# Performance work log

Hardware: AMD Instinct MI355X
Metric: run time of the kernel (lower is better)

## Reference

```python
import jax, jax.numpy as jnp
import numpy as np

N, M, F, W = 600000, 300000, 128, 256  # points, masked points, grid feat_dim, net width


def _lin_init(k, fi, fo):
    k1, k2 = jax.random.split(k)
    s = 1.0 / np.sqrt(fi)
    return (jax.random.uniform(k1, (fi, fo), jnp.float32, -s, s),
            jax.random.uniform(k2, (fo,), jnp.float32, -s, s))


def setup_inputs() -> dict:
    key = jax.random.key(0)
    ks = jax.random.split(key, 24)
    # unique sorted indices emulate the boolean target_mask (static count M)
    idx = jnp.asarray(np.sort(np.random.RandomState(0).permutation(N)[:M]).astype(np.int32))
    inp = {
        "rays_pts_emb": jax.random.normal(ks[0], (N, 3), jnp.float32),
        "rotations_emb": jax.random.normal(ks[1], (N, 4), jnp.float32),
        "shs_emb": jax.random.normal(ks[2], (N, 16, 3), jnp.float32),
        "time_emb": jax.random.uniform(ks[3], (N, 1), jnp.float32),
        "h_emb": jax.random.uniform(ks[4], (N, 1), jnp.float32),
        "grid_sp": jax.random.normal(ks[5], (M, F), jnp.float32),
        "grid_st": jax.random.normal(ks[6], (M, F), jnp.float32),
        "idx": idx,
    }
    layers = [("sp", F, W), ("st", F, W), ("p1", W, W), ("p2", W, 9),
              ("r1", W, W), ("r2", W, 4), ("s1", W, W), ("s2", W, 48),
              ("w1", W, W), ("w2", W, 1), ("m1", W, W), ("m2", W, 1)]
    for i, (nm, fi, fo) in enumerate(layers):
        Wt, b = _lin_init(ks[7 + i], fi, fo)
        inp["W_" + nm] = Wt
        inp["b_" + nm] = b
    return inp


def _head(x, W1, b1, W2, b2):
    # nn.Sequential(ReLU, Linear, ReLU, Linear)
    h = jax.nn.relu(x)
    h = jax.nn.relu(h @ W1 + b1)
    return h @ W2 + b2


def reference(rays_pts_emb, rotations_emb, shs_emb, time_emb, h_emb, grid_sp, grid_st, idx,
              W_sp, b_sp, W_st, b_st, W_p1, b_p1, W_p2, b_p2, W_r1, b_r1, W_r2, b_r2,
              W_s1, b_s1, W_s2, b_s2, W_w1, b_w1, W_w2, b_w2, W_m1, b_m1, W_m2, b_m2):
    # encoders (Linear only, no activation)
    sp = grid_sp @ W_sp + b_sp            # [M, W]
    st = grid_st @ W_st + b_st            # [M, W]
    t = time_emb[0:1]                     # [1, 1]
    mint = 1.0 - t
    # position deformation: Bezier combination of 3 control offsets
    dx = _head(sp, W_p1, b_p1, W_p2, b_p2).reshape(-1, 3, 3)  # [M, 3, 3]
    delta = (3.0 * mint ** 2 * t * dx[:, 0]
             + 3.0 * mint * t ** 2 * dx[:, 1]
             + t ** 3 * dx[:, 2])                              # [M, 3]
    pts = rays_pts_emb.at[idx].add(delta)
    rotations = rotations_emb.at[idx].add(_head(st, W_r1, b_r1, W_r2, b_r2))
    shs = shs_emb.at[idx].add(_head(st, W_s1, b_s1, W_s2, b_s2).reshape(-1, 16, 3))
    # opacity gating
    w = _head(sp, W_w1, b_w1, W_w2, b_w2) ** 2                 # [M, 1]
    mu = jax.nn.sigmoid(_head(sp, W_m1, b_m1, W_m2, b_m2))     # [M, 1]
    opacity = h_emb.at[idx].set(h_emb[idx] * jnp.exp(-w * (t - mu) ** 2))
    return (pts, rotations, opacity, shs)
```

## Files before the change

### kernel.cpp

```cpp
#include <hip/hip_runtime.h>
#include <hip/hip_bf16.h>
#include <stdint.h>

#define M_ROWS 300000

typedef __attribute__((ext_vector_type(8)))  short bf16x8;
typedef __attribute__((ext_vector_type(16))) float f32x16;

union U4 { uint4 u; bf16x8 h; unsigned short us[8]; };

__device__ __forceinline__ unsigned short f2bf(float f) {
  union { float f; uint32_t u; } v; v.f = f;
  uint32_t r = v.u + 0x7fffu + ((v.u >> 16) & 1u);
  return (unsigned short)(r >> 16);
}
__device__ __forceinline__ uint32_t pk2(float lo, float hi) {
  return (uint32_t)f2bf(lo) | ((uint32_t)f2bf(hi) << 16);
}

#define T_SP 0
#define T_ST 64
#define T_P1 128
#define T_P2 256
#define T_R1 272
#define T_R2 400
#define T_S1 416
#define T_S2 544
#define T_W1 576
#define T_W2 704
#define T_M1 720
#define T_M2 848
#define T_TOT 864

__global__ void prep_w(const float* Wsp, const float* Wst, const float* Wp1, const float* Wp2,
                       const float* Wr1, const float* Wr2, const float* Ws1, const float* Ws2,
                       const float* Ww1, const float* Ww2, const float* Wm1, const float* Wm2,
                       uint4* ws) {
  int b = blockIdx.x, l = threadIdx.x;
  const int starts[12] = {T_SP,T_ST,T_P1,T_P2,T_R1,T_R2,T_S1,T_S2,T_W1,T_W2,T_M1,T_M2};
  const int Ks[12]     = {128,128,256,256,256,256,256,256,256,256,256,256};
  const int Cos[12]    = {256,256,256,9,256,4,256,48,256,1,256,1};
  const float* Wp[12]  = {Wsp,Wst,Wp1,Wp2,Wr1,Wr2,Ws1,Ws2,Ww1,Ww2,Wm1,Wm2};
  int m = 0;
  #pragma unroll
  for (int i = 1; i < 12; ++i) if (b >= starts[i]) m = i;
  int local = b - starts[m];
  int KT = Ks[m] >> 4;
  int n0 = local / KT, k0 = local - n0 * KT;
  int col = n0 * 32 + (l & 31);
  int kbase = k0 * 16 + (l >> 5) * 8;
  const float* W = Wp[m];
  int Co = Cos[m];
  U4 pk;
  #pragma unroll
  for (int j = 0; j < 8; ++j) {
    float v = (col < Co) ? W[(size_t)(kbase + j) * Co + col] : 0.0f;
    pk.us[j] = f2bf(v);
  }
  ws[(size_t)b * 64 + l] = pk.u;
}

__global__ void copy_emb(const float4* pts, const float4* rot, const float4* h,
                         const float4* shs, float4* out) {
  long long stride = (long long)gridDim.x * blockDim.x;
  for (long long i = (long long)blockIdx.x * blockDim.x + threadIdx.x; i < 8400000LL; i += stride) {
    float4 v;
    if (i < 450000)        v = pts[i];
    else if (i < 1050000)  v = rot[i - 450000];
    else if (i < 1200000)  v = h[i - 1050000];
    else                   v = shs[i - 1200000];
    out[i] = v;
  }
}

#define LSTR 512
__device__ __forceinline__ int lds_addr(int row, int cb) {
  return row * LSTR + (cb ^ ((row & 15) << 4));
}

__device__ __forceinline__ void loadX(const float* grid, int row0, int t, char* buf) {
  #pragma unroll
  for (int i = 0; i < 4; ++i) {
    int fi = i * 512 + t;
    int row = fi >> 5;
    int c4 = fi & 31;
    int gr = row0 + row; gr = gr < M_ROWS ? gr : (M_ROWS - 1);
    float4 v = ((const float4*)grid)[(size_t)gr * 32 + c4];
    ushort4 p;
    p.x = f2bf(v.x); p.y = f2bf(v.y); p.z = f2bf(v.z); p.w = f2bf(v.w);
    *(ushort4*)(buf + lds_addr(row, c4 * 8)) = p;
  }
}

__device__ __forceinline__ void pre8(U4 (&d)[8], const uint4* base, int lane) {
  #pragma unroll
  for (int i = 0; i < 8; ++i) d[i].u = base[(size_t)i * 64 + lane];
}
__device__ __forceinline__ void pre4(U4 (&d)[8], const uint4* base, int lane) {
  #pragma unroll
  for (int i = 0; i < 4; ++i) d[i].u = base[(size_t)i * 64 + lane];
}
__device__ __forceinline__ void pre_s2(U4 (&d)[8], const uint4* wt, int kq, int lane) {
  #pragma unroll
  for (int kk = 0; kk < 4; ++kk)
    #pragma unroll
    for (int n = 0; n < 2; ++n)
      d[kk * 2 + n].u = wt[(size_t)((n * 16 + kq * 4 + kk) * 64) + lane];
}

__device__ __forceinline__ void mm_big8T(U4 (&b)[8], const char* inb, int k0, int arow, int khalf,
                                         f32x16& acc0, f32x16& acc1) {
  #pragma unroll
  for (int k = 0; k < 8; ++k) {
    bf16x8 x0 = *(const bf16x8*)(inb + lds_addr(arow, (k0 + k) * 32 + khalf));
    bf16x8 x1 = *(const bf16x8*)(inb + lds_addr(32 + arow, (k0 + k) * 32 + khalf));
    acc0 = __builtin_amdgcn_mfma_f32_32x32x16_bf16(b[k].h, x0, acc0, 0, 0, 0);
    acc1 = __builtin_amdgcn_mfma_f32_32x32x16_bf16(b[k].h, x1, acc1, 0, 0, 0);
  }
}

__device__ __forceinline__ void store_actT(char* outb, const float* bias, int wave, int lane,
                                           const f32x16& acc0, const f32x16& acc1) {
  const int xr = lane & 31;
  const int cb0 = wave * 32 + 4 * (lane >> 5);
  #pragma unroll
  for (int run = 0; run < 4; ++run) {
    const int c0 = cb0 + 8 * run;
    const float4 bv = *(const float4*)(bias + c0);
    uint2 w0, w1;
    w0.x = pk2(fmaxf(acc0[run * 4 + 0] + bv.x, 0.0f), fmaxf(acc0[run * 4 + 1] + bv.y, 0.0f));
    w0.y = pk2(fmaxf(acc0[run * 4 + 2] + bv.z, 0.0f), fmaxf(acc0[run * 4 + 3] + bv.w, 0.0f));
    w1.x = pk2(fmaxf(acc1[run * 4 + 0] + bv.x, 0.0f), fmaxf(acc1[run * 4 + 1] + bv.y, 0.0f));
    w1.y = pk2(fmaxf(acc1[run * 4 + 2] + bv.z, 0.0f), fmaxf(acc1[run * 4 + 3] + bv.w, 0.0f));
    *(uint2*)(outb + lds_addr(xr, c0 * 2)) = w0;
    *(uint2*)(outb + lds_addr(32 + xr, c0 * 2)) = w1;
  }
}

__device__ __forceinline__ void mm_head1(U4 (&b)[8], const char* inb, int rg, int kq, int khalf,
                                         int lane, f32x16& acc) {
  const int arow = rg * 32 + (lane & 31);
  #pragma unroll
  for (int kk = 0; kk < 4; ++kk) {
    bf16x8 a = *(const bf16x8*)(inb + lds_addr(arow, (kq * 4 + kk) * 32 + khalf));
    acc = __builtin_amdgcn_mfma_f32_32x32x16_bf16(a, b[kk].h, acc, 0, 0, 0);
  }
}

template<int COLS>
__device__ __forceinline__ void head_atomic(float* outsm, int rg, int lane, const f32x16& acc) {
  int col = lane & 31;
  if (col < COLS) {
    #pragma unroll
    for (int q = 0; q < 16; ++q) {
      int row = rg * 32 + (q & 3) + 8 * (q >> 2) + 4 * (lane >> 5);
      atomicAdd(&outsm[row * COLS + col], acc[q]);
    }
  }
}
__device__ __forceinline__ void head_atomic48(float* outsm, int rg, int lane,
                                              const f32x16& a0, const f32x16& a1) {
  int c = lane & 31;
  #pragma unroll
  for (int q = 0; q < 16; ++q) {
    int row = rg * 32 + (q & 3) + 8 * (q >> 2) + 4 * (lane >> 5);
    atomicAdd(&outsm[row * 48 + c], a0[q]);
    if (c < 16) atomicAdd(&outsm[row * 48 + 32 + c], a1[q]);
  }
}

__global__ void __launch_bounds__(512, 4) deform_main(
    const float* grid_sp, const float* grid_st, const int* idx,
    const float* rays, const float* rotq, const float* shs_in,
    const float* time_emb, const float* h_emb,
    const uint4* ws,
    const float* b_sp, const float* b_st, const float* b_p1, const float* b_p2,
    const float* b_r1, const float* b_r2, const float* b_s1, const float* b_s2,
    const float* b_w1, const float* b_w2, const float* b_m1, const float* b_m2,
    float* out) {
  __shared__ char bufA[32768];
  __shared__ char bufB[32768];
  __shared__ float smf[3456];
  __shared__ int sidx[64];
  float* dxb  = smf;
  float* shsb = smf;
  float* wb   = smf + 3072;
  float* mub  = smf + 3136;
  float* rotb = smf + 3200;

  const int t = threadIdx.x;
  const int lane = t & 63;
  const int wave = t >> 6;
  const int rg = wave & 1;
  const int kq = wave >> 1;
  const int arow = lane & 31;
  const int khalf = (lane >> 5) * 16;
  const int row0 = blockIdx.x * 64;
  const float tt = time_emb[0];

  U4 b0[8], b1[8];
  pre8(b0, ws + (size_t)(T_SP + wave * 8) * 64, lane);

  if (t < 64) { int gr = row0 + t; sidx[t] = idx[gr < M_ROWS ? gr : (M_ROWS - 1)]; }
  for (int i = t; i < 576; i += 512) dxb[i] = 0.0f;
  for (int i = 3072 + t; i < 3456; i += 512) smf[i] = 0.0f;
  loadX(grid_sp, row0, t, bufA);
  __syncthreads();

  {
    f32x16 a0 = (f32x16)0.0f, a1 = (f32x16)0.0f;
    pre8(b1, ws + (size_t)(T_P1 + wave * 16) * 64, lane);
    mm_big8T(b0, bufA, 0, arow, khalf, a0, a1);
    store_actT(bufB, b_sp, wave, lane, a0, a1);
  }
  __syncthreads();

  {
    f32x16 a0 = (f32x16)0.0f, a1 = (f32x16)0.0f;
    pre8(b0, ws + (size_t)(T_P1 + wave * 16 + 8) * 64, lane);
    mm_big8T(b1, bufB, 0, arow, khalf, a0, a1);
    pre4(b1, ws + (size_t)(T_P2 + kq * 4) * 64, lane);
    mm_big8T(b0, bufB, 8, arow, khalf, a0, a1);
    store_actT(bufA, b_p1, wave, lane, a0, a1);
  }
  __syncthreads();

  {
    f32x16 hacc = (f32x16)0.0f;
    pre8(b0, ws + (size_t)(T_W1 + wave * 16) * 64, lane);
    mm_head1(b1, bufA, rg, kq, khalf, lane, hacc);
    head_atomic<9>(dxb, rg, lane, hacc);
  }
  __syncthreads();

  {
    f32x16 a0 = (f32x16)0.0f, a1 = (f32x16)0.0f;
    pre8(b1, ws + (size_t)(T_W1 + wave * 16 + 8) * 64, lane);
    mm_big8T(b0, bufB, 0, arow, khalf, a0, a1);
    pre4(b0, ws + (size_t)(T_W2 + kq * 4) * 64, lane);
    mm_big8T(b1, bufB, 8, arow, khalf, a0, a1);
    store_actT(bufA, b_w1, wave, lane, a0, a1);
  }
  __syncthreads();

  {
    f32x16 hacc = (f32x16)0.0f;
    pre8(b1, ws + (size_t)(T_M1 + wave * 16) * 64, lane);
    mm_head1(b0, bufA, rg, kq, khalf, lane, hacc);
    head_atomic<1>(wb, rg, lane, hacc);
  }
  __syncthreads();

  {
    f32x16 a0 = (f32x16)0.0f, a1 = (f32x16)0.0f;
    pre8(b0, ws + (size_t)(T_M1 + wave * 16 + 8) * 64, lane);
    mm_big8T(b1, bufB, 0, arow, khalf, a0, a1);
    pre4(b1, ws + (size_t)(T_M2 + kq * 4) * 64, lane);
    mm_big8T(b0, bufB, 8, arow, khalf, a0, a1);
    store_actT(bufA, b_m1, wave, lane, a0, a1);
  }
  __syncthreads();

  float pr = 0.0f, hv = 0.0f;
  {
    if (t < 256) {
      int row = t >> 2, sub = t & 3;
      int g = sidx[row];
      if (sub < 3) pr = rays[(size_t)g * 3 + sub]; else hv = h_emb[g];
    }
    loadX(grid_st, row0, t, bufB);
    f32x16 hacc = (f32x16)0.0f;
    mm_head1(b1, bufA, rg, kq, khalf, lane, hacc);
    pre8(b0, ws + (size_t)(T_ST + wave * 8) * 64, lane);
    head_atomic<1>(mub, rg, lane, hacc);
  }
  __syncthreads();

  {
    f32x16 a0 = (f32x16)0.0f, a1 = (f32x16)0.0f;
    pre8(b1, ws + (size_t)(T_R1 + wave * 16) * 64, lane);
    mm_big8T(b0, bufB, 0, arow, khalf, a0, a1);
    store_actT(bufA, b_st, wave, lane, a0, a1);
    if (t < 256) {
      int row = t >> 2, sub = t & 3;
      int gr = row0 + row;
      if (gr < M_ROWS) {
        int g = sidx[row];
        if (sub < 3) {
          float mt = 1.0f - tt;
          float c0 = 3.0f * mt * mt * tt, c1 = 3.0f * mt * tt * tt, c2 = tt * tt * tt;
          float d0 = dxb[row * 9 + sub]     + b_p2[sub];
          float d1 = dxb[row * 9 + 3 + sub] + b_p2[3 + sub];
          float d2 = dxb[row * 9 + 6 + sub] + b_p2[6 + sub];
          out[(size_t)g * 3 + sub] = pr + (c0 * d0 + c1 * d1 + c2 * d2);
        } else {
          float wr = wb[row] + b_w2[0];
          float mr = mub[row] + b_m2[0];
          float mu = 1.0f / (1.0f + expf(-mr));
          float dtm = tt - mu;
          out[4200000 + (size_t)g] = hv * expf(-(wr * wr) * dtm * dtm);
        }
      }
    }
  }
  __syncthreads();

  {
    f32x16 a0 = (f32x16)0.0f, a1 = (f32x16)0.0f;
    pre8(b0, ws + (size_t)(T_R1 + wave * 16 + 8) * 64, lane);
    mm_big8T(b1, bufA, 0, arow, khalf, a0, a1);
    pre4(b1, ws + (size_t)(T_R2 + kq * 4) * 64, lane);
    mm_big8T(b0, bufA, 8, arow, khalf, a0, a1);
    store_actT(bufB, b_r1, wave, lane, a0, a1);
  }
  __syncthreads();

  float4 rq;
  {
    if (t < 64) rq = ((const float4*)rotq)[sidx[t]];
    f32x16 hacc = (f32x16)0.0f;
    mm_head1(b1, bufB, rg, kq, khalf, lane, hacc);
    pre8(b0, ws + (size_t)(T_S1 + wave * 16) * 64, lane);
    #pragma unroll
    for (int i = 0; i < 6; ++i) shsb[i * 512 + t] = 0.0f;
    head_atomic<4>(rotb, rg, lane, hacc);
  }
  __syncthreads();

  {
    f32x16 a0 = (f32x16)0.0f, a1 = (f32x16)0.0f;
    pre8(b1, ws + (size_t)(T_S1 + wave * 16 + 8) * 64, lane);
    mm_big8T(b0, bufA, 0, arow, khalf, a0, a1);
    pre_s2(b0, ws + (size_t)T_S2 * 64, kq, lane);
    mm_big8T(b1, bufA, 8, arow, khalf, a0, a1);
    store_actT(bufB, b_s1, wave, lane, a0, a1);
    if (t < 64 && row0 + t < M_ROWS) {
      int g = sidx[t];
      float4 o;
      o.x = rq.x + rotb[t * 4 + 0] + b_r2[0];
      o.y = rq.y + rotb[t * 4 + 1] + b_r2[1];
      o.z = rq.z + rotb[t * 4 + 2] + b_r2[2];
      o.w = rq.w + rotb[t * 4 + 3] + b_r2[3];
      ((float4*)out)[450000 + (size_t)g] = o;
    }
  }
  __syncthreads();

  float4 sv0, sv1;
  int r0v = t / 12, c40 = t - r0v * 12;
  int e1 = 512 + t, r1v = e1 / 12, c41 = e1 - r1v * 12;
  {
    sv0 = ((const float4*)shs_in)[(size_t)sidx[r0v] * 12 + c40];
    if (t < 256) sv1 = ((const float4*)shs_in)[(size_t)sidx[r1v] * 12 + c41];
    f32x16 h0 = (f32x16)0.0f, h1 = (f32x16)0.0f;
    const int ar = rg * 32 + (lane & 31);
    #pragma unroll
    for (int kk = 0; kk < 4; ++kk) {
      bf16x8 a = *(const bf16x8*)(bufB + lds_addr(ar, (kq * 4 + kk) * 32 + khalf));
      h0 = __builtin_amdgcn_mfma_f32_32x32x16_bf16(a, b0[kk * 2 + 0].h, h0, 0, 0, 0);
      h1 = __builtin_amdgcn_mfma_f32_32x32x16_bf16(a, b0[kk * 2 + 1].h, h1, 0, 0, 0);
    }
    head_atomic48(shsb, rg, lane, h0, h1);
  }
  __syncthreads();

  {
    if (row0 + r0v < M_ROWS) {
      float4 bias0 = ((const float4*)b_s2)[c40];
      float4 acc0 = ((const float4*)shsb)[r0v * 12 + c40];
      float4 o;
      o.x = sv0.x + acc0.x + bias0.x; o.y = sv0.y + acc0.y + bias0.y;
      o.z = sv0.z + acc0.z + bias0.z; o.w = sv0.w + acc0.w + bias0.w;
      ((float4*)out)[1200000 + (size_t)sidx[r0v] * 12 + c40] = o;
    }
    if (t < 256 && row0 + r1v < M_ROWS) {
      float4 bias1 = ((const float4*)b_s2)[c41];
      float4 acc1 = ((const float4*)shsb)[r1v * 12 + c41];
      float4 o;
      o.x = sv1.x + acc1.x + bias1.x; o.y = sv1.y + acc1.y + bias1.y;
      o.z = sv1.z + acc1.z + bias1.z; o.w = sv1.w + acc1.w + bias1.w;
      ((float4*)out)[1200000 + (size_t)sidx[r1v] * 12 + c41] = o;
    }
  }
}

extern "C" void kernel_launch(void* const* d_in, const int* in_sizes, int n_in,
                              void* d_out, int out_size, void* d_ws, size_t ws_size,
                              hipStream_t stream) {
  const float* rays     = (const float*)d_in[0];
  const float* rotq     = (const float*)d_in[1];
  const float* shs      = (const float*)d_in[2];
  const float* time_emb = (const float*)d_in[3];
  const float* h_emb    = (const float*)d_in[4];
  const float* grid_sp  = (const float*)d_in[5];
  const float* grid_st  = (const float*)d_in[6];
  const int*   idx      = (const int*)d_in[7];
  uint4* ws = (uint4*)d_ws;

  prep_w<<<T_TOT, 64, 0, stream>>>(
      (const float*)d_in[8],  (const float*)d_in[10], (const float*)d_in[12], (const float*)d_in[14],
      (const float*)d_in[16], (const float*)d_in[18], (const float*)d_in[20], (const float*)d_in[22],
      (const float*)d_in[24], (const float*)d_in[26], (const float*)d_in[28], (const float*)d_in[30],
      ws);

  copy_emb<<<2048, 256, 0, stream>>>((const float4*)rays, (const float4*)rotq,
                                     (const float4*)h_emb, (const float4*)shs, (float4*)d_out);

  deform_main<<<(M_ROWS + 63) / 64, 512, 0, stream>>>(
      grid_sp, grid_st, idx, rays, rotq, shs, time_emb, h_emb, ws,
      (const float*)d_in[9],  (const float*)d_in[11], (const float*)d_in[13], (const float*)d_in[15],
      (const float*)d_in[17], (const float*)d_in[19], (const float*)d_in[21], (const float*)d_in[23],
      (const float*)d_in[25], (const float*)d_in[27], (const float*)d_in[29], (const float*)d_in[31],
      (float*)d_out);
}
```

Measured before the change: 769.5 us.

## Fuse width-one opacity heads into register reductions and merge barrier stages

The w and mu heads end in a 256-to-1 linear layer. They now skip writing the hidden activation to LDS and skip the second MFMA pass. Each lane instead applies bias and ReLU, dots its columns with the fp32 output weights, and atomically adds partial sums into shared memory. Several stages are merged to drop __syncthreads barriers: the dx head, the w/mu layer-1 matmuls, the rotation stage and the shs layer-1 matmul. This cuts LDS traffic and synchronisation but keeps more accumulators live, which raises register pressure, and it adds LDS atomic contention with 16 waves contributing per row.

```diff
diff --git a/kernel.cpp b/kernel.cpp
--- a/kernel.cpp
+++ b/kernel.cpp
@@ -137,6 +137,28 @@
   }
 }
 
+__device__ __forceinline__ void fused_head1(const f32x16& a0, const f32x16& a1,
+                                            const float* bias, const float* w2,
+                                            int wave, int lane, float* outsm) {
+  const int cb0 = wave * 32 + 4 * (lane >> 5);
+  float p0 = 0.0f, p1 = 0.0f;
+  #pragma unroll
+  for (int run = 0; run < 4; ++run) {
+    const float4 bv = *(const float4*)(bias + cb0 + 8 * run);
+    const float4 wv = *(const float4*)(w2 + cb0 + 8 * run);
+    p0 += fmaxf(a0[run * 4 + 0] + bv.x, 0.0f) * wv.x;
+    p0 += fmaxf(a0[run * 4 + 1] + bv.y, 0.0f) * wv.y;
+    p0 += fmaxf(a0[run * 4 + 2] + bv.z, 0.0f) * wv.z;
+    p0 += fmaxf(a0[run * 4 + 3] + bv.w, 0.0f) * wv.w;
+    p1 += fmaxf(a1[run * 4 + 0] + bv.x, 0.0f) * wv.x;
+    p1 += fmaxf(a1[run * 4 + 1] + bv.y, 0.0f) * wv.y;
+    p1 += fmaxf(a1[run * 4 + 2] + bv.z, 0.0f) * wv.z;
+    p1 += fmaxf(a1[run * 4 + 3] + bv.w, 0.0f) * wv.w;
+  }
+  atomicAdd(&outsm[lane & 31], p0);
+  atomicAdd(&outsm[32 + (lane & 31)], p1);
+}
+
 __device__ __forceinline__ void mm_head1(U4 (&b)[8], const char* inb, int rg, int kq, int khalf,
                                          int lane, f32x16& acc) {
   const int arow = rg * 32 + (lane & 31);
@@ -173,7 +195,7 @@
     const float* grid_sp, const float* grid_st, const int* idx,
     const float* rays, const float* rotq, const float* shs_in,
     const float* time_emb, const float* h_emb,
-    const uint4* ws,
+    const uint4* ws, const float* Ww2f, const float* Wm2f,
     const float* b_sp, const float* b_st, const float* b_p1, const float* b_p2,
     const float* b_r1, const float* b_r2, const float* b_s1, const float* b_s2,
     const float* b_w1, const float* b_w2, const float* b_m1, const float* b_m2,
@@ -225,42 +247,6 @@
   }
   __syncthreads();
 
-  {
-    f32x16 hacc = (f32x16)0.0f;
-    pre8(b0, ws + (size_t)(T_W1 + wave * 16) * 64, lane);
-    mm_head1(b1, bufA, rg, kq, khalf, lane, hacc);
-    head_atomic<9>(dxb, rg, lane, hacc);
-  }
-  __syncthreads();
-
-  {
-    f32x16 a0 = (f32x16)0.0f, a1 = (f32x16)0.0f;
-    pre8(b1, ws + (size_t)(T_W1 + wave * 16 + 8) * 64, lane);
-    mm_big8T(b0, bufB, 0, arow, khalf, a0, a1);
-    pre4(b0, ws + (size_t)(T_W2 + kq * 4) * 64, lane);
-    mm_big8T(b1, bufB, 8, arow, khalf, a0, a1);
-    store_actT(bufA, b_w1, wave, lane, a0, a1);
-  }
-  __syncthreads();
-
-  {
-    f32x16 hacc = (f32x16)0.0f;
-    pre8(b1, ws + (size_t)(T_M1 + wave * 16) * 64, lane);
-    mm_head1(b0, bufA, rg, kq, khalf, lane, hacc);
-    head_atomic<1>(wb, rg, lane, hacc);
-  }
-  __syncthreads();
-
-  {
-    f32x16 a0 = (f32x16)0.0f, a1 = (f32x16)0.0f;
-    pre8(b0, ws + (size_t)(T_M1 + wave * 16 + 8) * 64, lane);
-    mm_big8T(b1, bufB, 0, arow, khalf, a0, a1);
-    pre4(b1, ws + (size_t)(T_M2 + kq * 4) * 64, lane);
-    mm_big8T(b0, bufB, 8, arow, khalf, a0, a1);
-    store_actT(bufA, b_m1, wave, lane, a0, a1);
-  }
-  __syncthreads();
-
   float pr = 0.0f, hv = 0.0f;
   {
     if (t < 256) {
@@ -268,11 +254,46 @@
       int g = sidx[row];
       if (sub < 3) pr = rays[(size_t)g * 3 + sub]; else hv = h_emb[g];
     }
-    loadX(grid_st, row0, t, bufB);
+    pre8(b0, ws + (size_t)(T_W1 + wave * 16) * 64, lane);
     f32x16 hacc = (f32x16)0.0f;
     mm_head1(b1, bufA, rg, kq, khalf, lane, hacc);
+    head_atomic<9>(dxb, rg, lane, hacc);
+    f32x16 a0 = (f32x16)0.0f, a1 = (f32x16)0.0f;
+    pre8(b1, ws + (size_t)(T_W1 + wave * 16 + 8) * 64, lane);
+    mm_big8T(b0, bufB, 0, arow, khalf, a0, a1);
+    pre8(b0, ws + (size_t)(T_M1 + wave * 16) * 64, lane);
+    mm_big8T(b1, bufB, 8, arow, khalf, a0, a1);
+    fused_head1(a0, a1, b_w1, Ww2f, wave, lane, wb);
+    a0 = (f32x16)0.0f; a1 = (f32x16)0.0f;
+    pre8(b1, ws + (size_t)(T_M1 + wave * 16 + 8) * 64, lane);
+    mm_big8T(b0, bufB, 0, arow, khalf, a0, a1);
     pre8(b0, ws + (size_t)(T_ST + wave * 8) * 64, lane);
-    head_atomic<1>(mub, rg, lane, hacc);
+    mm_big8T(b1, bufB, 8, arow, khalf, a0, a1);
+    fused_head1(a0, a1, b_m1, Wm2f, wave, lane, mub);
+  }
+  __syncthreads();
+
+  loadX(grid_st, row0, t, bufB);
+  if (t < 256) {
+    int row = t >> 2, sub = t & 3;
+    int gr = row0 + row;
+    if (gr < M_ROWS) {
+      int g = sidx[row];
+      if (sub < 3) {
+        float mt = 1.0f - tt;
+        float c0 = 3.0f * mt * mt * tt, c1 = 3.0f * mt * tt * tt, c2 = tt * tt * tt;
+        float d0 = dxb[row * 9 + sub]     + b_p2[sub];
+        float d1 = dxb[row * 9 + 3 + sub] + b_p2[3 + sub];
+        float d2 = dxb[row * 9 + 6 + sub] + b_p2[6 + sub];
+        out[(size_t)g * 3 + sub] = pr + (c0 * d0 + c1 * d1 + c2 * d2);
+      } else {
+        float wr = wb[row] + b_w2[0];
+        float mr = mub[row] + b_m2[0];
+        float mu = 1.0f / (1.0f + expf(-mr));
+        float dtm = tt - mu;
+        out[4200000 + (size_t)g] = hv * expf(-(wr * wr) * dtm * dtm);
+      }
+    }
   }
   __syncthreads();
 
@@ -281,59 +302,38 @@
     pre8(b1, ws + (size_t)(T_R1 + wave * 16) * 64, lane);
     mm_big8T(b0, bufB, 0, arow, khalf, a0, a1);
     store_actT(bufA, b_st, wave, lane, a0, a1);
-    if (t < 256) {
-      int row = t >> 2, sub = t & 3;
-      int gr = row0 + row;
-      if (gr < M_ROWS) {
-        int g = sidx[row];
-        if (sub < 3) {
-          float mt = 1.0f - tt;
-          float c0 = 3.0f * mt * mt * tt, c1 = 3.0f * mt * tt * tt, c2 = tt * tt * tt;
-          float d0 = dxb[row * 9 + sub]     + b_p2[sub];
-          float d1 = dxb[row * 9 + 3 + sub] + b_p2[3 + sub];
-          float d2 = dxb[row * 9 + 6 + sub] + b_p2[6 + sub];
-          out[(size_t)g * 3 + sub] = pr + (c0 * d0 + c1 * d1 + c2 * d2);
-        } else {
-          float wr = wb[row] + b_w2[0];
-          float mr = mub[row] + b_m2[0];
-          float mu = 1.0f / (1.0f + expf(-mr));
-          float dtm = tt - mu;
-          out[4200000 + (size_t)g] = hv * expf(-(wr * wr) * dtm * dtm);
-        }
-      }
-    }
-  }
-  __syncthreads();
-
-  {
+  }
+  __syncthreads();
+
+  float4 rq;
+  {
+    if (t < 64) rq = ((const float4*)rotq)[sidx[t]];
     f32x16 a0 = (f32x16)0.0f, a1 = (f32x16)0.0f;
     pre8(b0, ws + (size_t)(T_R1 + wave * 16 + 8) * 64, lane);
     mm_big8T(b1, bufA, 0, arow, khalf, a0, a1);
     pre4(b1, ws + (size_t)(T_R2 + kq * 4) * 64, lane);
     mm_big8T(b0, bufA, 8, arow, khalf, a0, a1);
     store_actT(bufB, b_r1, wave, lane, a0, a1);
-  }
-  __syncthreads();
-
-  float4 rq;
-  {
-    if (t < 64) rq = ((const float4*)rotq)[sidx[t]];
+    #pragma unroll
+    for (int i = 0; i < 6; ++i) shsb[i * 512 + t] = 0.0f;
+  }
+  __syncthreads();
+
+  f32x16 s0 = (f32x16)0.0f, s1 = (f32x16)0.0f;
+  {
+    pre8(b0, ws + (size_t)(T_S1 + wave * 16) * 64, lane);
     f32x16 hacc = (f32x16)0.0f;
     mm_head1(b1, bufB, rg, kq, khalf, lane, hacc);
-    pre8(b0, ws + (size_t)(T_S1 + wave * 16) * 64, lane);
-    #pragma unroll
-    for (int i = 0; i < 6; ++i) shsb[i * 512 + t] = 0.0f;
     head_atomic<4>(rotb, rg, lane, hacc);
-  }
-  __syncthreads();
-
-  {
-    f32x16 a0 = (f32x16)0.0f, a1 = (f32x16)0.0f;
     pre8(b1, ws + (size_t)(T_S1 + wave * 16 + 8) * 64, lane);
-    mm_big8T(b0, bufA, 0, arow, khalf, a0, a1);
+    mm_big8T(b0, bufA, 0, arow, khalf, s0, s1);
     pre_s2(b0, ws + (size_t)T_S2 * 64, kq, lane);
-    mm_big8T(b1, bufA, 8, arow, khalf, a0, a1);
-    store_actT(bufB, b_s1, wave, lane, a0, a1);
+    mm_big8T(b1, bufA, 8, arow, khalf, s0, s1);
+  }
+  __syncthreads();
+
+  {
+    store_actT(bufB, b_s1, wave, lane, s0, s1);
     if (t < 64 && row0 + t < M_ROWS) {
       int g = sidx[t];
       float4 o;
@@ -408,6 +408,7 @@
 
   deform_main<<<(M_ROWS + 63) / 64, 512, 0, stream>>>(
       grid_sp, grid_st, idx, rays, rotq, shs, time_emb, h_emb, ws,
+      (const float*)d_in[26], (const float*)d_in[30],
       (const float*)d_in[9],  (const float*)d_in[11], (const float*)d_in[13], (const float*)d_in[15],
       (const float*)d_in[17], (const float*)d_in[19], (const float*)d_in[21], (const float*)d_in[23],
       (const float*)d_in[25], (const float*)d_in[27], (const float*)d_in[29], (const float*)d_in[31],
```

After: 1.039 ms. +35.1%, slower.

## Accumulate rotation and SH head outputs with global atomics and raise MFMA priority

Applied to the files above, without the earlier changes.

The rotation and SH head partial sums from the four K-split waves are now added with atomicAdd directly into the global output, with the bias folded in by the first K-slice. This replaces the LDS staging buffers, their zeroing, the gathers of rotq and shs_in, two barriers and the final store pass, and shrinks shared memory from about 3.4K to 704 floats. It relies on the output already holding a copy of the input rotations and SH coefficients, and it issues several times more scattered global atomics than the plain stores it replaces. Every MFMA loop is also wrapped in s_setprio raise and lower calls, so waves issuing matrix work get scheduling priority.

```diff
diff --git a/kernel.cpp b/kernel.cpp
--- a/kernel.cpp
+++ b/kernel.cpp
@@ -158,14 +158,38 @@
     }
   }
 }
-__device__ __forceinline__ void head_atomic48(float* outsm, int rg, int lane,
-                                              const f32x16& a0, const f32x16& a1) {
+
+__device__ __forceinline__ void rot_atomic_global(const f32x16& acc, int rg, int kq, int lane,
+                                                  const int* sidx, int row0, const float* b_r2,
+                                                  float* out) {
+  int col = lane & 31;
+  if (col < 4) {
+    float bb = (kq == 0) ? b_r2[col] : 0.0f;
+    #pragma unroll
+    for (int q = 0; q < 16; ++q) {
+      int row = rg * 32 + (q & 3) + 8 * (q >> 2) + 4 * (lane >> 5);
+      if (row0 + row < M_ROWS) {
+        atomicAdd(out + 1800000 + (size_t)sidx[row] * 4 + col, acc[q] + bb);
+      }
+    }
+  }
+}
+
+__device__ __forceinline__ void shs_atomic_global(const f32x16& a0, const f32x16& a1,
+                                                  int rg, int kq, int lane,
+                                                  const int* sidx, int row0, const float* b_s2,
+                                                  float* out) {
   int c = lane & 31;
+  float bb0 = (kq == 0) ? b_s2[c] : 0.0f;
+  float bb1 = (kq == 0 && c < 16) ? b_s2[32 + c] : 0.0f;
   #pragma unroll
   for (int q = 0; q < 16; ++q) {
     int row = rg * 32 + (q & 3) + 8 * (q >> 2) + 4 * (lane >> 5);
-    atomicAdd(&outsm[row * 48 + c], a0[q]);
-    if (c < 16) atomicAdd(&outsm[row * 48 + 32 + c], a1[q]);
+    if (row0 + row < M_ROWS) {
+      size_t base = 4800000 + (size_t)sidx[row] * 48;
+      atomicAdd(out + base + c, a0[q] + bb0);
+      if (c < 16) atomicAdd(out + base + 32 + c, a1[q] + bb1);
+    }
   }
 }
 
@@ -180,13 +204,11 @@
     float* out) {
   __shared__ char bufA[32768];
   __shared__ char bufB[32768];
-  __shared__ float smf[3456];
+  __shared__ float smf[704];
   __shared__ int sidx[64];
-  float* dxb  = smf;
-  float* shsb = smf;
-  float* wb   = smf + 3072;
-  float* mub  = smf + 3136;
-  float* rotb = smf + 3200;
+  float* dxb = smf;
+  float* wb  = smf + 576;
+  float* mub = smf + 640;
 
   const int t = threadIdx.x;
   const int lane = t & 63;
@@ -202,15 +224,17 @@
   pre8(b0, ws + (size_t)(T_SP + wave * 8) * 64, lane);
 
   if (t < 64) { int gr = row0 + t; sidx[t] = idx[gr < M_ROWS ? gr : (M_ROWS - 1)]; }
-  for (int i = t; i < 576; i += 512) dxb[i] = 0.0f;
-  for (int i = 3072 + t; i < 3456; i += 512) smf[i] = 0.0f;
+  if (t < 512) smf[t] = 0.0f;
+  if (t < 192) smf[512 + t] = 0.0f;
   loadX(grid_sp, row0, t, bufA);
   __syncthreads();
 
   {
     f32x16 a0 = (f32x16)0.0f, a1 = (f32x16)0.0f;
     pre8(b1, ws + (size_t)(T_P1 + wave * 16) * 64, lane);
+    __builtin_amdgcn_s_setprio(1);
     mm_big8T(b0, bufA, 0, arow, khalf, a0, a1);
+    __builtin_amdgcn_s_setprio(0);
     store_actT(bufB, b_sp, wave, lane, a0, a1);
   }
   __syncthreads();
@@ -218,9 +242,13 @@
   {
     f32x16 a0 = (f32x16)0.0f, a1 = (f32x16)0.0f;
     pre8(b0, ws + (size_t)(T_P1 + wave * 16 + 8) * 64, lane);
+    __builtin_amdgcn_s_setprio(1);
     mm_big8T(b1, bufB, 0, arow, khalf, a0, a1);
+    __builtin_amdgcn_s_setprio(0);
     pre4(b1, ws + (size_t)(T_P2 + kq * 4) * 64, lane);
+    __builtin_amdgcn_s_setprio(1);
     mm_big8T(b0, bufB, 8, arow, khalf, a0, a1);
+    __builtin_amdgcn_s_setprio(0);
     store_actT(bufA, b_p1, wave, lane, a0, a1);
   }
   __syncthreads();
@@ -228,7 +256,9 @@
   {
     f32x16 hacc = (f32x16)0.0f;
     pre8(b0, ws + (size_t)(T_W1 + wave * 16) * 64, lane);
+    __builtin_amdgcn_s_setprio(1);
     mm_head1(b1, bufA, rg, kq, khalf, lane, hacc);
+    __builtin_amdgcn_s_setprio(0);
     head_atomic<9>(dxb, rg, lane, hacc);
   }
   __syncthreads();
@@ -236,9 +266,13 @@
   {
     f32x16 a0 = (f32x16)0.0f, a1 = (f32x16)0.0f;
     pre8(b1, ws + (size_t)(T_W1 + wave * 16 + 8) * 64, lane);
+    __builtin_amdgcn_s_setprio(1);
     mm_big8T(b0, bufB, 0, arow, khalf, a0, a1);
+    __builtin_amdgcn_s_setprio(0);
     pre4(b0, ws + (size_t)(T_W2 + kq * 4) * 64, lane);
+    __builtin_amdgcn_s_setprio(1);
     mm_big8T(b1, bufB, 8, arow, khalf, a0, a1);
+    __builtin_amdgcn_s_setprio(0);
     store_actT(bufA, b_w1, wave, lane, a0, a1);
   }
   __syncthreads();
@@ -246,7 +280,9 @@
   {
     f32x16 hacc = (f32x16)0.0f;
     pre8(b1, ws + (size_t)(T_M1 + wave * 16) * 64, lane);
+    __builtin_amdgcn_s_setprio(1);
     mm_head1(b0, bufA, rg, kq, khalf, lane, hacc);
+    __builtin_amdgcn_s_setprio(0);
     head_atomic<1>(wb, rg, lane, hacc);
   }
   __syncthreads();
@@ -254,9 +290,13 @@
   {
     f32x16 a0 = (f32x16)0.0f, a1 = (f32x16)0.0f;
     pre8(b0, ws + (size_t)(T_M1 + wave * 16 + 8) * 64, lane);
+    __builtin_amdgcn_s_setprio(1);
     mm_big8T(b1, bufB, 0, arow, khalf, a0, a1);
+    __builtin_amdgcn_s_setprio(0);
     pre4(b1, ws + (size_t)(T_M2 + kq * 4) * 64, lane);
+    __builtin_amdgcn_s_setprio(1);
     mm_big8T(b0, bufB, 8, arow, khalf, a0, a1);
+    __builtin_amdgcn_s_setprio(0);
     store_actT(bufA, b_m1, wave, lane, a0, a1);
   }
   __syncthreads();
@@ -270,7 +310,9 @@
     }
     loadX(grid_st, row0, t, bufB);
     f32x16 hacc = (f32x16)0.0f;
+    __builtin_amdgcn_s_setprio(1);
     mm_head1(b1, bufA, rg, kq, khalf, lane, hacc);
+    __builtin_amdgcn_s_setprio(0);
     pre8(b0, ws + (size_t)(T_ST + wave * 8) * 64, lane);
     head_atomic<1>(mub, rg, lane, hacc);
   }
@@ -279,7 +321,9 @@
   {
     f32x16 a0 = (f32x16)0.0f, a1 = (f32x16)0.0f;
     pre8(b1, ws + (size_t)(T_R1 + wave * 16) * 64, lane);
+    __builtin_amdgcn_s_setprio(1);
     mm_big8T(b0, bufB, 0, arow, khalf, a0, a1);
+    __builtin_amdgcn_s_setprio(0);
     store_actT(bufA, b_st, wave, lane, a0, a1);
     if (t < 256) {
       int row = t >> 2, sub = t & 3;
@@ -308,79 +352,53 @@
   {
     f32x16 a0 = (f32x16)0.0f, a1 = (f32x16)0.0f;
     pre8(b0, ws + (size_t)(T_R1 + wave * 16 + 8) * 64, lane);
+    __builtin_amdgcn_s_setprio(1);
     mm_big8T(b1, bufA, 0, arow, khalf, a0, a1);
+    __builtin_amdgcn_s_setprio(0);
     pre4(b1, ws + (size_t)(T_R2 + kq * 4) * 64, lane);
+    __builtin_amdgcn_s_setprio(1);
     mm_big8T(b0, bufA, 8, arow, khalf, a0, a1);
+    __builtin_amdgcn_s_setprio(0);
     store_actT(bufB, b_r1, wave, lane, a0, a1);
   }
   __syncthreads();
 
-  float4 rq;
-  {
-    if (t < 64) rq = ((const float4*)rotq)[sidx[t]];
+  {
     f32x16 hacc = (f32x16)0.0f;
+    pre8(b0, ws + (size_t)(T_S1 + wave * 16) * 64, lane);
+    __builtin_amdgcn_s_setprio(1);
     mm_head1(b1, bufB, rg, kq, khalf, lane, hacc);
-    pre8(b0, ws + (size_t)(T_S1 + wave * 16) * 64, lane);
-    #pragma unroll
-    for (int i = 0; i < 6; ++i) shsb[i * 512 + t] = 0.0f;
-    head_atomic<4>(rotb, rg, lane, hacc);
+    __builtin_amdgcn_s_setprio(0);
+    rot_atomic_global(hacc, rg, kq, lane, sidx, row0, b_r2, out);
   }
   __syncthreads();
 
   {
     f32x16 a0 = (f32x16)0.0f, a1 = (f32x16)0.0f;
     pre8(b1, ws + (size_t)(T_S1 + wave * 16 + 8) * 64, lane);
+    __builtin_amdgcn_s_setprio(1);
     mm_big8T(b0, bufA, 0, arow, khalf, a0, a1);
+    __builtin_amdgcn_s_setprio(0);
     pre_s2(b0, ws + (size_t)T_S2 * 64, kq, lane);
+    __builtin_amdgcn_s_setprio(1);
     mm_big8T(b1, bufA, 8, arow, khalf, a0, a1);
+    __builtin_amdgcn_s_setprio(0);
     store_actT(bufB, b_s1, wave, lane, a0, a1);
-    if (t < 64 && row0 + t < M_ROWS) {
-      int g = sidx[t];
-      float4 o;
-      o.x = rq.x + rotb[t * 4 + 0] + b_r2[0];
-      o.y = rq.y + rotb[t * 4 + 1] + b_r2[1];
-      o.z = rq.z + rotb[t * 4 + 2] + b_r2[2];
-      o.w = rq.w + rotb[t * 4 + 3] + b_r2[3];
-      ((float4*)out)[450000 + (size_t)g] = o;
-    }
-  }
-  __syncthreads();
-
-  float4 sv0, sv1;
-  int r0v = t / 12, c40 = t - r0v * 12;
-  int e1 = 512 + t, r1v = e1 / 12, c41 = e1 - r1v * 12;
-  {
-    sv0 = ((const float4*)shs_in)[(size_t)sidx[r0v] * 12 + c40];
-    if (t < 256) sv1 = ((const float4*)shs_in)[(size_t)sidx[r1v] * 12 + c41];
+  }
+  __syncthreads();
+
+  {
     f32x16 h0 = (f32x16)0.0f, h1 = (f32x16)0.0f;
     const int ar = rg * 32 + (lane & 31);
+    __builtin_amdgcn_s_setprio(1);
     #pragma unroll
     for (int kk = 0; kk < 4; ++kk) {
       bf16x8 a = *(const bf16x8*)(bufB + lds_addr(ar, (kq * 4 + kk) * 32 + khalf));
       h0 = __builtin_amdgcn_mfma_f32_32x32x16_bf16(a, b0[kk * 2 + 0].h, h0, 0, 0, 0);
       h1 = __builtin_amdgcn_mfma_f32_32x32x16_bf16(a, b0[kk * 2 + 1].h, h1, 0, 0, 0);
     }
-    head_atomic48(shsb, rg, lane, h0, h1);
-  }
-  __syncthreads();
-
-  {
-    if (row0 + r0v < M_ROWS) {
-      float4 bias0 = ((const float4*)b_s2)[c40];
-      float4 acc0 = ((const float4*)shsb)[r0v * 12 + c40];
-      float4 o;
-      o.x = sv0.x + acc0.x + bias0.x; o.y = sv0.y + acc0.y + bias0.y;
-      o.z = sv0.z + acc0.z + bias0.z; o.w = sv0.w + acc0.w + bias0.w;
-      ((float4*)out)[1200000 + (size_t)sidx[r0v] * 12 + c40] = o;
-    }
-    if (t < 256 && row0 + r1v < M_ROWS) {
-      float4 bias1 = ((const float4*)b_s2)[c41];
-      float4 acc1 = ((const float4*)shsb)[r1v * 12 + c41];
-      float4 o;
-      o.x = sv1.x + acc1.x + bias1.x; o.y = sv1.y + acc1.y + bias1.y;
-      o.z = sv1.z + acc1.z + bias1.z; o.w = sv1.w + acc1.w + bias1.w;
-      ((float4*)out)[1200000 + (size_t)sidx[r1v] * 12 + c41] = o;
-    }
+    __builtin_amdgcn_s_setprio(0);
+    shs_atomic_global(h0, h1, rg, kq, lane, sidx, row0, b_s2, out);
   }
 }
 
```

New measurement: 741.0 us, median of 2. 1.04x faster.
